# Kernel tuning notes

Measured on AMD Instinct MI355X. Metric: run time of the kernel, lower is better.

Reference implementation:

```python
import jax, jax.numpy as jnp
import numpy as np

B, S, H = 1, 2048, 4608
NH, NKV, HD = 36, 4, 128
GROUP = NH // NKV  # 9
ROPE_THETA = 100000.0
SLIDING_WINDOW = 1024


def _rope_tables(seq_len, head_dim):
    inv_freq = 1.0 / (ROPE_THETA ** (jnp.arange(0, head_dim, 2, dtype=jnp.float32) / head_dim))
    ang = jnp.arange(seq_len, dtype=jnp.float32)[:, None] * inv_freq[None, :]  # [S, HD/2]
    emb = jnp.concatenate([ang, ang], axis=-1)  # [S, HD]
    return jnp.cos(emb), jnp.sin(emb)


def setup_inputs() -> dict:
    key = jax.random.key(0)
    ks = jax.random.split(key, 10)
    std = 0.02
    cos_table, sin_table = _rope_tables(S, HD)
    return {
        "hidden_states": jax.random.normal(ks[0], (B, S, H), jnp.float32),
        "position_ids": jnp.broadcast_to(jnp.arange(S, dtype=jnp.int64)[None, :], (B, S)),
        "cos_table": cos_table,
        "sin_table": sin_table,
        "q_w": jax.random.normal(ks[1], (NH * HD, H), jnp.float32) * std,
        "q_b": jax.random.normal(ks[2], (NH * HD,), jnp.float32) * std,
        "k_w": jax.random.normal(ks[3], (NKV * HD, H), jnp.float32) * std,
        "k_b": jax.random.normal(ks[4], (NKV * HD,), jnp.float32) * std,
        "v_w": jax.random.normal(ks[5], (NKV * HD, H), jnp.float32) * std,
        "v_b": jax.random.normal(ks[6], (NKV * HD,), jnp.float32) * std,
        "o_w": jax.random.normal(ks[7], (H, NH * HD), jnp.float32) * std,
        "o_b": jax.random.normal(ks[8], (H,), jnp.float32) * std,
        "sliding_window": SLIDING_WINDOW,
    }


def _rotate_half(x):
    x1, x2 = jnp.split(x, 2, axis=-1)
    return jnp.concatenate([-x2, x1], axis=-1)


def reference(hidden_states, position_ids, cos_table, sin_table,
              q_w, q_b, k_w, k_b, v_w, v_b, o_w, o_b, sliding_window):
    bsz, q_len, _ = hidden_states.shape
    scaling = HD ** -0.5

    q = (hidden_states @ q_w.T + q_b).reshape(bsz, q_len, NH, HD)
    k = (hidden_states @ k_w.T + k_b).reshape(bsz, q_len, NKV, HD)
    v = (hidden_states @ v_w.T + v_b).reshape(bsz, q_len, NKV, HD)

    # RoPE with explicit cos/sin, unsqueeze_dim=2 ('bsnd' layout)
    cos = cos_table[position_ids][:, :, None, :]  # [B, S, 1, HD]
    sin = sin_table[position_ids][:, :, None, :]
    q = q * cos + _rotate_half(q) * sin
    k = k * cos + _rotate_half(k) * sin

    # GQA: group Q heads per KV head
    qg = q.reshape(bsz, q_len, NKV, GROUP, HD)
    logits = jnp.einsum('bqgrd,bkgd->bgrqk', qg, k) * scaling  # [B, NKV, GROUP, S, S]

    # causal + sliding-window mask: attend where k <= q and q - k < window
    idx = jnp.arange(q_len)
    mask = (idx[:, None] >= idx[None, :]) & (idx[:, None] - idx[None, :] < sliding_window)
    logits = jnp.where(mask[None, None, None, :, :], logits, jnp.finfo(logits.dtype).min)

    probs = jax.nn.softmax(logits, axis=-1)
    attn = jnp.einsum('bgrqk,bkgd->bqgrd', probs, v).reshape(bsz, q_len, NH * HD)
    return attn @ o_w.T + o_b
```

## Files before the change

### kernel.cpp

```cpp
#include <hip/hip_runtime.h>
#include <stdint.h>

typedef __attribute__((ext_vector_type(8))) __bf16 bf16x8;
typedef __attribute__((ext_vector_type(4))) float f32x4;
typedef __attribute__((ext_vector_type(8))) unsigned short u16x8;
typedef __attribute__((ext_vector_type(4))) unsigned short u16x4;

#define SEQ 2048
#define HID 4608
#define NQKV 5632
#define NHEAD 36
#define NKVH 4
#define HDIM 128
#define WINDOW 1024

__device__ __forceinline__ unsigned short f2b(float f) {
    unsigned u = __builtin_bit_cast(unsigned, f);
    u += 0x7fffu + ((u >> 16) & 1u);
    return (unsigned short)(u >> 16);
}
__device__ __forceinline__ float b2f(unsigned short h) {
    unsigned u = ((unsigned)h) << 16;
    return __builtin_bit_cast(float, u);
}

#define GLD16(gp, lp) __builtin_amdgcn_global_load_lds( \
    (const __attribute__((address_space(1))) void*)(gp), \
    (__attribute__((address_space(3))) void*)(lp), 16, 0, 0)

#define VMCNT8() asm volatile("s_waitcnt vmcnt(8)" ::: "memory")
#define VMCNT0() asm volatile("s_waitcnt vmcnt(0)" ::: "memory")
#define BARRIER() asm volatile("s_barrier" ::: "memory")

__global__ __launch_bounds__(256) void conv_kernel(const float* __restrict__ src,
                                                   unsigned short* __restrict__ dst, int n4) {
    int stride = gridDim.x * blockDim.x;
    for (int i = blockIdx.x * blockDim.x + threadIdx.x; i < n4; i += stride) {
        float4 v = ((const float4*)src)[i];
        ushort4 o;
        o.x = f2b(v.x); o.y = f2b(v.y); o.z = f2b(v.z); o.w = f2b(v.w);
        ((ushort4*)dst)[i] = o;
    }
}

__global__ __launch_bounds__(512, 2) void gemm256_kernel(
    const unsigned short* __restrict__ A,
    const unsigned short* __restrict__ W,
    void* __restrict__ out,
    const float* __restrict__ b0, const float* __restrict__ b1, const float* __restrict__ b2,
    int N, int K, int GX, int outf32)
{
    __shared__ alignas(16) unsigned short lds[2][2][256 * 64];

    const int tid = threadIdx.x;
    const int w = tid >> 6, lane = tid & 63;
    const int r16 = lane & 15, kg = lane >> 4;
    const int wm = w >> 2, wn = w & 3;

    const int cpx = gridDim.x >> 3;
    const int o = blockIdx.x;
    const int id = (o & 7) * cpx + (o >> 3);
    const int bx = id % GX, by = id / GX;
    const int row0 = by * 256, col0 = bx * 256;

    const int lr = lane >> 3;
    const int lc = lane & 7;
    const int cg = lc ^ lr;
    const unsigned short* aP[4];
    const unsigned short* bP[4];
#pragma unroll
    for (int j = 0; j < 4; ++j) {
        const int L = w * 4 + j;
        aP[j] = A + (size_t)(row0 + L * 8 + lr) * K + cg * 8;
        bP[j] = W + (size_t)(col0 + L * 8 + lr) * K + cg * 8;
    }

    const int NT = K >> 6;
    f32x4 acc[8][4] = {};

#pragma unroll
    for (int j = 0; j < 4; ++j) GLD16(aP[j], (char*)&lds[0][0][0] + (w * 4 + j) * 1024);
#pragma unroll
    for (int j = 0; j < 4; ++j) GLD16(bP[j], (char*)&lds[0][1][0] + (w * 4 + j) * 1024);
#pragma unroll
    for (int j = 0; j < 4; ++j) { aP[j] += 64; bP[j] += 64; }

    const int swz = r16 & 7;
    for (int t = 0; t < NT; ++t) {
        const int cur = t & 1;
        if (t + 1 < NT) {
            const int nxt = cur ^ 1;
#pragma unroll
            for (int j = 0; j < 4; ++j) GLD16(aP[j], (char*)&lds[nxt][0][0] + (w * 4 + j) * 1024);
#pragma unroll
            for (int j = 0; j < 4; ++j) GLD16(bP[j], (char*)&lds[nxt][1][0] + (w * 4 + j) * 1024);
#pragma unroll
            for (int j = 0; j < 4; ++j) { aP[j] += 64; bP[j] += 64; }
            VMCNT8();
        } else {
            VMCNT0();
        }
        BARRIER();

        const unsigned short* As_ = &lds[cur][0][0];
        const unsigned short* Bs_ = &lds[cur][1][0];

        bf16x8 af[4][2], bf0[2][2], bf1[2][2];
#pragma unroll
        for (int ni = 0; ni < 2; ++ni)
#pragma unroll
            for (int kh = 0; kh < 2; ++kh) {
                int rb0 = wn * 64 + ni * 16 + r16;
                int rb1 = wn * 64 + 32 + ni * 16 + r16;
                bf0[ni][kh] = *(const bf16x8*)(Bs_ + rb0 * 64 + ((kh * 4 + kg) ^ swz) * 8);
                bf1[ni][kh] = *(const bf16x8*)(Bs_ + rb1 * 64 + ((kh * 4 + kg) ^ swz) * 8);
            }
#pragma unroll
        for (int mi = 0; mi < 4; ++mi)
#pragma unroll
            for (int kh = 0; kh < 2; ++kh) {
                int ra = wm * 128 + mi * 16 + r16;
                af[mi][kh] = *(const bf16x8*)(As_ + ra * 64 + ((kh * 4 + kg) ^ swz) * 8);
            }

        __builtin_amdgcn_s_setprio(1);
#pragma unroll
        for (int mi = 0; mi < 4; ++mi)
#pragma unroll
            for (int ni = 0; ni < 2; ++ni)
#pragma unroll
                for (int kh = 0; kh < 2; ++kh)
                    acc[mi][ni] = __builtin_amdgcn_mfma_f32_16x16x32_bf16(af[mi][kh], bf0[ni][kh], acc[mi][ni], 0, 0, 0);
        __builtin_amdgcn_s_setprio(0);
        __builtin_amdgcn_s_setprio(1);
#pragma unroll
        for (int mi = 0; mi < 4; ++mi)
#pragma unroll
            for (int ni = 0; ni < 2; ++ni)
#pragma unroll
                for (int kh = 0; kh < 2; ++kh)
                    acc[mi][2 + ni] = __builtin_amdgcn_mfma_f32_16x16x32_bf16(af[mi][kh], bf1[ni][kh], acc[mi][2 + ni], 0, 0, 0);
        __builtin_amdgcn_s_setprio(0);
#pragma unroll
        for (int mi = 0; mi < 4; ++mi)
#pragma unroll
            for (int kh = 0; kh < 2; ++kh) {
                int ra = wm * 128 + 64 + mi * 16 + r16;
                af[mi][kh] = *(const bf16x8*)(As_ + ra * 64 + ((kh * 4 + kg) ^ swz) * 8);
            }
        __builtin_amdgcn_s_setprio(1);
#pragma unroll
        for (int mi = 0; mi < 4; ++mi)
#pragma unroll
            for (int ni = 0; ni < 2; ++ni)
#pragma unroll
                for (int kh = 0; kh < 2; ++kh)
                    acc[4 + mi][2 + ni] = __builtin_amdgcn_mfma_f32_16x16x32_bf16(af[mi][kh], bf1[ni][kh], acc[4 + mi][2 + ni], 0, 0, 0);
        __builtin_amdgcn_s_setprio(0);
        __builtin_amdgcn_s_setprio(1);
#pragma unroll
        for (int mi = 0; mi < 4; ++mi)
#pragma unroll
            for (int ni = 0; ni < 2; ++ni)
#pragma unroll
                for (int kh = 0; kh < 2; ++kh)
                    acc[4 + mi][ni] = __builtin_amdgcn_mfma_f32_16x16x32_bf16(af[mi][kh], bf0[ni][kh], acc[4 + mi][ni], 0, 0, 0);
        __builtin_amdgcn_s_setprio(0);

        BARRIER();
    }

    if (!outf32) {
        unsigned short* O = (unsigned short*)out;
#pragma unroll
        for (int m = 0; m < 8; ++m)
#pragma unroll
            for (int n = 0; n < 4; ++n)
#pragma unroll
                for (int r = 0; r < 4; ++r) {
                    int row = row0 + wm * 128 + m * 16 + kg * 4 + r;
                    int col = col0 + wn * 64 + n * 16 + r16;
                    float bias = (col < HID) ? b0[col]
                               : (col < HID + 512 ? b1[col - HID] : b2[col - HID - 512]);
                    O[(size_t)row * N + col] = f2b(acc[m][n][r] + bias);
                }
    } else {
        float* O = (float*)out;
#pragma unroll
        for (int m = 0; m < 8; ++m)
#pragma unroll
            for (int n = 0; n < 4; ++n)
#pragma unroll
                for (int r = 0; r < 4; ++r) {
                    int row = row0 + wm * 128 + m * 16 + kg * 4 + r;
                    int col = col0 + wn * 64 + n * 16 + r16;
                    O[(size_t)row * N + col] = acc[m][n][r] + b0[col];
                }
    }
}

__global__ __launch_bounds__(256) void rope_kernel(unsigned short* __restrict__ qkv,
                                                   const float* __restrict__ cos_t,
                                                   const float* __restrict__ sin_t) {
    int idx = blockIdx.x * 256 + threadIdx.x;
    int d = idx & 63;
    int t = idx >> 6;
    int head = t % 40;
    int s = t / 40;
    int base = head < NHEAD ? head * HDIM : HID + (head - NHEAD) * HDIM;
    size_t off = (size_t)s * NQKV + base;
    float x = b2f(qkv[off + d]);
    float y = b2f(qkv[off + d + 64]);
    float c = cos_t[s * HDIM + d];
    float sn = sin_t[s * HDIM + d];
    qkv[off + d]      = f2b(x * c - y * sn);
    qkv[off + d + 64] = f2b(y * c + x * sn);
}

__global__ __launch_bounds__(256) void vtrans_kernel(const unsigned short* __restrict__ qkv,
                                                     unsigned short* __restrict__ vtg) {
    __shared__ unsigned short tile[32][36];
    const int s0 = blockIdx.x * 32, d0 = blockIdx.y * 32, kvh = blockIdx.z;
    const int lid = threadIdx.x;
    {
        int sl = lid >> 3, dc = (lid & 7) * 4;
        u16x4 v = *(const u16x4*)(qkv + (size_t)(s0 + sl) * NQKV + HID + 512 + kvh * HDIM + d0 + dc);
#pragma unroll
        for (int i = 0; i < 4; ++i) tile[sl][dc + i] = v[i];
    }
    __syncthreads();
    {
        int dl = lid >> 3, sc = (lid & 7) * 4;
        u16x4 v;
#pragma unroll
        for (int i = 0; i < 4; ++i) v[i] = tile[sc + i][dl];
        *(u16x4*)(vtg + (size_t)kvh * HDIM * SEQ + (size_t)(d0 + dl) * SEQ + s0 + sc) = v;
    }
}

#define KSTR 136
#define VSTR 72
#define PSTR 88
__global__ __launch_bounds__(256) void attn_kernel(const unsigned short* __restrict__ qkv,
                                                   const unsigned short* __restrict__ vtg,
                                                   unsigned short* __restrict__ aout)
{
    __shared__ alignas(16) unsigned short Ks[64 * KSTR];
    __shared__ alignas(16) unsigned short Vt[128 * VSTR];
    __shared__ alignas(16) unsigned short Ps[4 * 16 * PSTR];
    const int h = blockIdx.x, qb = blockIdx.y;
    const int q0 = qb * 64;
    const int kvh = h / 9;
    const int tid = threadIdx.x, wid = tid >> 6, lane = tid & 63;
    const int r16 = lane & 15, kg = lane >> 4;
    const int qbase = q0 + wid * 16;
    const unsigned short* vsrc = vtg + (size_t)kvh * HDIM * SEQ;

    bf16x8 qf[4];
    {
        const unsigned short* qrow = qkv + (size_t)(qbase + r16) * NQKV + h * HDIM;
#pragma unroll
        for (int kk = 0; kk < 4; ++kk)
            qf[kk] = *(const bf16x8*)(qrow + kk * 32 + kg * 8);
    }

    f32x4 o[8] = {};
    float mrow[4], lrow[4];
#pragma unroll
    for (int r = 0; r < 4; ++r) { mrow[r] = -1e30f; lrow[r] = 0.f; }

    int lo = q0 - (WINDOW - 1); if (lo < 0) lo = 0; lo &= ~63;
    unsigned short* myP = Ps + wid * 16 * PSTR;
    const float scale = 0.08838834764831845f;

    for (int kt = lo; kt <= q0; kt += 64) {
        for (int c = tid; c < 1024; c += 256) {
            int key = c >> 4, dc = c & 15;
            const unsigned short* kp = qkv + (size_t)(kt + key) * NQKV + HID + kvh * HDIM + dc * 8;
            *(u16x8*)(Ks + key * KSTR + dc * 8) = *(const u16x8*)kp;
            int d = c >> 3, k8 = (c & 7) * 8;
            *(u16x8*)(Vt + d * VSTR + k8) = *(const u16x8*)(vsrc + (size_t)d * SEQ + kt + k8);
        }
        __syncthreads();

        f32x4 sc[4] = {};
#pragma unroll
        for (int t = 0; t < 4; ++t)
#pragma unroll
            for (int kk = 0; kk < 4; ++kk) {
                bf16x8 kf = *(const bf16x8*)(Ks + (t * 16 + r16) * KSTR + kk * 32 + kg * 8);
                sc[t] = __builtin_amdgcn_mfma_f32_16x16x32_bf16(qf[kk], kf, sc[t], 0, 0, 0);
            }

        float p[4][4], mt[4];
#pragma unroll
        for (int r = 0; r < 4; ++r) mt[r] = -1e30f;
#pragma unroll
        for (int t = 0; t < 4; ++t)
#pragma unroll
            for (int r = 0; r < 4; ++r) {
                int q = qbase + kg * 4 + r;
                int key = kt + t * 16 + r16;
                bool valid = (key <= q) && (q - key < WINDOW);
                float v = valid ? sc[t][r] * scale : -1e30f;
                p[t][r] = v;
                mt[r] = fmaxf(mt[r], v);
            }
#pragma unroll
        for (int mask = 1; mask <= 8; mask <<= 1)
#pragma unroll
            for (int r = 0; r < 4; ++r)
                mt[r] = fmaxf(mt[r], __shfl_xor(mt[r], mask, 64));

        float alpha[4], tsum[4];
#pragma unroll
        for (int r = 0; r < 4; ++r) {
            float mnew = fmaxf(mrow[r], mt[r]);
            alpha[r] = __expf(mrow[r] - mnew);
            mrow[r] = mnew;
            tsum[r] = 0.f;
        }
#pragma unroll
        for (int t = 0; t < 4; ++t)
#pragma unroll
            for (int r = 0; r < 4; ++r) {
                float e = __expf(p[t][r] - mrow[r]);
                p[t][r] = e;
                tsum[r] += e;
            }
#pragma unroll
        for (int mask = 1; mask <= 8; mask <<= 1)
#pragma unroll
            for (int r = 0; r < 4; ++r)
                tsum[r] += __shfl_xor(tsum[r], mask, 64);
#pragma unroll
        for (int r = 0; r < 4; ++r)
            lrow[r] = lrow[r] * alpha[r] + tsum[r];
#pragma unroll
        for (int n = 0; n < 8; ++n)
#pragma unroll
            for (int r = 0; r < 4; ++r)
                o[n][r] = o[n][r] * alpha[r];

#pragma unroll
        for (int t = 0; t < 4; ++t)
#pragma unroll
            for (int r = 0; r < 4; ++r)
                myP[(kg * 4 + r) * PSTR + t * 16 + r16] = f2b(p[t][r]);
        asm volatile("s_waitcnt lgkmcnt(0)" ::: "memory");

#pragma unroll
        for (int kc = 0; kc < 2; ++kc) {
            bf16x8 pa = *(const bf16x8*)(myP + r16 * PSTR + kc * 32 + kg * 8);
#pragma unroll
            for (int n = 0; n < 8; ++n) {
                bf16x8 vb = *(const bf16x8*)(Vt + (n * 16 + r16) * VSTR + kc * 32 + kg * 8);
                o[n] = __builtin_amdgcn_mfma_f32_16x16x32_bf16(pa, vb, o[n], 0, 0, 0);
            }
        }
        __syncthreads();
    }

#pragma unroll
    for (int n = 0; n < 8; ++n)
#pragma unroll
        for (int r = 0; r < 4; ++r) {
            int q = qbase + kg * 4 + r;
            aout[(size_t)q * HID + h * HDIM + n * 16 + r16] = f2b(o[n][r] / lrow[r]);
        }
}

extern "C" void kernel_launch(void* const* d_in, const int* in_sizes, int n_in,
                              void* d_out, int out_size, void* d_ws, size_t ws_size,
                              hipStream_t stream) {
    const float* hidden = (const float*)d_in[0];
    const float* cos_t = (const float*)d_in[2];
    const float* sin_t = (const float*)d_in[3];
    const float* q_w = (const float*)d_in[4];
    const float* q_b = (const float*)d_in[5];
    const float* k_w = (const float*)d_in[6];
    const float* k_b = (const float*)d_in[7];
    const float* v_w = (const float*)d_in[8];
    const float* v_b = (const float*)d_in[9];
    const float* o_w = (const float*)d_in[10];
    const float* o_b = (const float*)d_in[11];

    char* ws = (char*)d_ws;
    unsigned short* hbf  = (unsigned short*)ws;
    unsigned short* attn = hbf;
    unsigned short* wqkv = (unsigned short*)(ws + 18874368);
    unsigned short* vtg  = wqkv;
    unsigned short* wo   = (unsigned short*)(ws + 70778880);
    unsigned short* qkv  = (unsigned short*)(ws + 113246208);

    dim3 blk(256);
    conv_kernel<<<2048, blk, 0, stream>>>(hidden, hbf, (SEQ * HID) / 4);
    conv_kernel<<<2048, blk, 0, stream>>>(q_w, wqkv, (HID * HID) / 4);
    conv_kernel<<<2048, blk, 0, stream>>>(k_w, wqkv + (size_t)HID * HID, (512 * HID) / 4);
    conv_kernel<<<2048, blk, 0, stream>>>(v_w, wqkv + (size_t)5120 * HID, (512 * HID) / 4);
    conv_kernel<<<2048, blk, 0, stream>>>(o_w, wo, (HID * HID) / 4);

    gemm256_kernel<<<dim3(176), dim3(512), 0, stream>>>(hbf, wqkv, qkv, q_b, k_b, v_b, NQKV, HID, 22, 0);
    rope_kernel<<<(SEQ * 40 * 64) / 256, blk, 0, stream>>>(qkv, cos_t, sin_t);
    vtrans_kernel<<<dim3(SEQ / 32, HDIM / 32, NKVH), blk, 0, stream>>>(qkv, vtg);
    attn_kernel<<<dim3(NHEAD, SEQ / 64), blk, 0, stream>>>(qkv, vtg, attn);
    gemm256_kernel<<<dim3(144), dim3(512), 0, stream>>>(attn, wo, d_out, o_b, nullptr, nullptr, HID, HID, 18, 1);
}
```

Before: 449.2 us.

## Restructure GEMM main loop into barrier-interleaved 128-K ping-pong schedule

The bf16 GEMM main loop now handles 128 of K per iteration using two 64-wide LDS slots, kept as separate A and B arrays. Each quarter of the MFMA work sits between barriers, and its LDS fragment reads and half-tile global-to-LDS prefetches are spread across those phases with staged vmcnt waits. The aim is to overlap global loads and LDS reads with MFMA execution more finely than the earlier whole-tile double buffer. In exchange it adds many more s_barrier points per iteration and tighter reuse of LDS slots, which risks stalls or read-after-overwrite hazards if a wait is placed wrong.

```diff
diff --git a/kernel.cpp b/kernel.cpp
--- a/kernel.cpp
+++ b/kernel.cpp
@@ -29,6 +29,7 @@
     (__attribute__((address_space(3))) void*)(lp), 16, 0, 0)
 
 #define VMCNT8() asm volatile("s_waitcnt vmcnt(8)" ::: "memory")
+#define VMCNT4() asm volatile("s_waitcnt vmcnt(4)" ::: "memory")
 #define VMCNT0() asm volatile("s_waitcnt vmcnt(0)" ::: "memory")
 #define BARRIER() asm volatile("s_barrier" ::: "memory")
 
@@ -50,7 +51,8 @@
     const float* __restrict__ b0, const float* __restrict__ b1, const float* __restrict__ b2,
     int N, int K, int GX, int outf32)
 {
-    __shared__ alignas(16) unsigned short lds[2][2][256 * 64];
+    __shared__ alignas(16) unsigned short ldsA[2][256 * 64];
+    __shared__ alignas(16) unsigned short ldsB[2][256 * 64];
 
     const int tid = threadIdx.x;
     const int w = tid >> 6, lane = tid & 63;
@@ -66,107 +68,91 @@
     const int lr = lane >> 3;
     const int lc = lane & 7;
     const int cg = lc ^ lr;
-    const unsigned short* aP[4];
-    const unsigned short* bP[4];
-#pragma unroll
-    for (int j = 0; j < 4; ++j) {
-        const int L = w * 4 + j;
-        aP[j] = A + (size_t)(row0 + L * 8 + lr) * K + cg * 8;
-        bP[j] = W + (size_t)(col0 + L * 8 + lr) * K + cg * 8;
-    }
-
-    const int NT = K >> 6;
+    const unsigned short* Abase = A + (size_t)row0 * K;
+    const unsigned short* Wbase = W + (size_t)col0 * K;
+
+    auto STG = [&](const unsigned short* Mat, unsigned short* ldsSlot, int hf, int kb) {
+#pragma unroll
+        for (int j = 0; j < 2; ++j) {
+            int row = hf * 128 + (w * 2 + j) * 8 + lr;
+            GLD16(Mat + (size_t)row * K + kb + cg * 8,
+                  (char*)ldsSlot + hf * 16384 + (w * 2 + j) * 1024);
+        }
+    };
+
+    const int NITER = K >> 7;
     f32x4 acc[8][4] = {};
-
-#pragma unroll
-    for (int j = 0; j < 4; ++j) GLD16(aP[j], (char*)&lds[0][0][0] + (w * 4 + j) * 1024);
-#pragma unroll
-    for (int j = 0; j < 4; ++j) GLD16(bP[j], (char*)&lds[0][1][0] + (w * 4 + j) * 1024);
-#pragma unroll
-    for (int j = 0; j < 4; ++j) { aP[j] += 64; bP[j] += 64; }
-
     const int swz = r16 & 7;
-    for (int t = 0; t < NT; ++t) {
-        const int cur = t & 1;
-        if (t + 1 < NT) {
-            const int nxt = cur ^ 1;
-#pragma unroll
-            for (int j = 0; j < 4; ++j) GLD16(aP[j], (char*)&lds[nxt][0][0] + (w * 4 + j) * 1024);
-#pragma unroll
-            for (int j = 0; j < 4; ++j) GLD16(bP[j], (char*)&lds[nxt][1][0] + (w * 4 + j) * 1024);
-#pragma unroll
-            for (int j = 0; j < 4; ++j) { aP[j] += 64; bP[j] += 64; }
-            VMCNT8();
-        } else {
-            VMCNT0();
-        }
-        BARRIER();
-
-        const unsigned short* As_ = &lds[cur][0][0];
-        const unsigned short* Bs_ = &lds[cur][1][0];
-
-        bf16x8 af[4][2], bf0[2][2], bf1[2][2];
-#pragma unroll
-        for (int ni = 0; ni < 2; ++ni)
-#pragma unroll
-            for (int kh = 0; kh < 2; ++kh) {
-                int rb0 = wn * 64 + ni * 16 + r16;
-                int rb1 = wn * 64 + 32 + ni * 16 + r16;
-                bf0[ni][kh] = *(const bf16x8*)(Bs_ + rb0 * 64 + ((kh * 4 + kg) ^ swz) * 8);
-                bf1[ni][kh] = *(const bf16x8*)(Bs_ + rb1 * 64 + ((kh * 4 + kg) ^ swz) * 8);
-            }
-#pragma unroll
-        for (int mi = 0; mi < 4; ++mi)
-#pragma unroll
-            for (int kh = 0; kh < 2; ++kh) {
-                int ra = wm * 128 + mi * 16 + r16;
-                af[mi][kh] = *(const bf16x8*)(As_ + ra * 64 + ((kh * 4 + kg) ^ swz) * 8);
-            }
-
-        __builtin_amdgcn_s_setprio(1);
-#pragma unroll
-        for (int mi = 0; mi < 4; ++mi)
-#pragma unroll
-            for (int ni = 0; ni < 2; ++ni)
-#pragma unroll
-                for (int kh = 0; kh < 2; ++kh)
-                    acc[mi][ni] = __builtin_amdgcn_mfma_f32_16x16x32_bf16(af[mi][kh], bf0[ni][kh], acc[mi][ni], 0, 0, 0);
-        __builtin_amdgcn_s_setprio(0);
-        __builtin_amdgcn_s_setprio(1);
-#pragma unroll
-        for (int mi = 0; mi < 4; ++mi)
-#pragma unroll
-            for (int ni = 0; ni < 2; ++ni)
-#pragma unroll
-                for (int kh = 0; kh < 2; ++kh)
-                    acc[mi][2 + ni] = __builtin_amdgcn_mfma_f32_16x16x32_bf16(af[mi][kh], bf1[ni][kh], acc[mi][2 + ni], 0, 0, 0);
-        __builtin_amdgcn_s_setprio(0);
-#pragma unroll
-        for (int mi = 0; mi < 4; ++mi)
-#pragma unroll
-            for (int kh = 0; kh < 2; ++kh) {
-                int ra = wm * 128 + 64 + mi * 16 + r16;
-                af[mi][kh] = *(const bf16x8*)(As_ + ra * 64 + ((kh * 4 + kg) ^ swz) * 8);
-            }
-        __builtin_amdgcn_s_setprio(1);
-#pragma unroll
-        for (int mi = 0; mi < 4; ++mi)
-#pragma unroll
-            for (int ni = 0; ni < 2; ++ni)
-#pragma unroll
-                for (int kh = 0; kh < 2; ++kh)
-                    acc[4 + mi][2 + ni] = __builtin_amdgcn_mfma_f32_16x16x32_bf16(af[mi][kh], bf1[ni][kh], acc[4 + mi][2 + ni], 0, 0, 0);
-        __builtin_amdgcn_s_setprio(0);
-        __builtin_amdgcn_s_setprio(1);
-#pragma unroll
-        for (int mi = 0; mi < 4; ++mi)
-#pragma unroll
-            for (int ni = 0; ni < 2; ++ni)
-#pragma unroll
-                for (int kh = 0; kh < 2; ++kh)
-                    acc[4 + mi][ni] = __builtin_amdgcn_mfma_f32_16x16x32_bf16(af[mi][kh], bf0[ni][kh], acc[4 + mi][ni], 0, 0, 0);
-        __builtin_amdgcn_s_setprio(0);
-
+
+    bf16x8 af[4][2], bfA[2][2], bfB[2][2];
+
+#define DSR_A(mh, Sl) \
+_Pragma("unroll") for (int mi = 0; mi < 4; ++mi) \
+_Pragma("unroll") for (int kh = 0; kh < 2; ++kh) \
+    af[mi][kh] = *(const bf16x8*)((Sl) + (wm * 128 + (mh) * 64 + mi * 16 + r16) * 64 + ((kh * 4 + kg) ^ swz) * 8);
+#define DSR_B(nh, Sl, BF) \
+_Pragma("unroll") for (int ni = 0; ni < 2; ++ni) \
+_Pragma("unroll") for (int kh = 0; kh < 2; ++kh) \
+    BF[ni][kh] = *(const bf16x8*)((Sl) + (wn * 64 + (nh) * 32 + ni * 16 + r16) * 64 + ((kh * 4 + kg) ^ swz) * 8);
+#define MFMA_Q(mh, nh, BF) \
+    __builtin_amdgcn_s_setprio(1); \
+_Pragma("unroll") for (int mi = 0; mi < 4; ++mi) \
+_Pragma("unroll") for (int ni = 0; ni < 2; ++ni) \
+_Pragma("unroll") for (int kh = 0; kh < 2; ++kh) \
+    acc[(mh) * 4 + mi][(nh) * 2 + ni] = __builtin_amdgcn_mfma_f32_16x16x32_bf16(af[mi][kh], BF[ni][kh], acc[(mh) * 4 + mi][(nh) * 2 + ni], 0, 0, 0); \
+    __builtin_amdgcn_s_setprio(0);
+
+    STG(Abase, ldsA[0], 0, 0);  STG(Abase, ldsA[0], 1, 0);
+    STG(Wbase, ldsB[0], 0, 0);  STG(Wbase, ldsB[0], 1, 0);
+    STG(Abase, ldsA[1], 0, 64); STG(Abase, ldsA[1], 1, 64);
+    STG(Wbase, ldsB[1], 0, 64); STG(Wbase, ldsB[1], 1, 64);
+    VMCNT0();
+    BARRIER();
+
+    for (int i = 0; i < NITER; ++i) {
+        const unsigned short* A0 = ldsA[0];
+        const unsigned short* B0 = ldsB[0];
+        const unsigned short* A1 = ldsA[1];
+        const unsigned short* B1 = ldsB[1];
+        const bool st = (i + 1 < NITER);
+        const int kb0 = (i + 1) * 128;
+        const int kb1 = kb0 + 64;
+
+        DSR_A(0, A0); DSR_B(0, B0, bfA);
+        BARRIER();
+        MFMA_Q(0, 0, bfA);
+        BARRIER();
+        DSR_B(1, B0, bfB);
+        BARRIER();
+        MFMA_Q(0, 1, bfB);
+        BARRIER();
+        DSR_A(1, A0);
+        if (st) STG(Wbase, ldsB[0], 0, kb0);
+        BARRIER();
+        MFMA_Q(1, 1, bfB);
+        BARRIER();
+        if (st) { STG(Abase, ldsA[0], 0, kb0); VMCNT4(); } else { VMCNT0(); }
+        BARRIER();
+        MFMA_Q(1, 0, bfA);
+        BARRIER();
+        DSR_A(0, A1); DSR_B(0, B1, bfA);
+        if (st) STG(Abase, ldsA[0], 1, kb0);
+        BARRIER();
+        MFMA_Q(0, 0, bfA);
+        BARRIER();
+        DSR_B(1, B1, bfB);
+        if (st) STG(Wbase, ldsB[0], 1, kb0);
+        BARRIER();
+        MFMA_Q(0, 1, bfB);
+        BARRIER();
+        DSR_A(1, A1);
+        if (st) { STG(Wbase, ldsB[1], 0, kb1); STG(Wbase, ldsB[1], 1, kb1); }
+        BARRIER();
+        MFMA_Q(1, 1, bfB);
+        BARRIER();
+        if (st) { STG(Abase, ldsA[1], 0, kb1); STG(Abase, ldsA[1], 1, kb1); VMCNT8(); }
+        BARRIER();
+        MFMA_Q(1, 0, bfA);
         BARRIER();
     }
 
@@ -197,6 +183,9 @@
                     O[(size_t)row * N + col] = acc[m][n][r] + b0[col];
                 }
     }
+#undef DSR_A
+#undef DSR_B
+#undef MFMA_Q
 }
 
 __global__ __launch_bounds__(256) void rope_kernel(unsigned short* __restrict__ qkv,
```

After: 444.5 us. No clear change (-1.0%).
